# Performance work log

Measured on AMD Instinct MI355X. Metric: run time of the kernel, lower is better.

The kernel has to match this reference:

```python
import jax, jax.numpy as jnp
from jax import lax
import numpy as np


def conv2d(x, w, b, stride=1, pad=0):
    # x: [B,C,H,W], w: [O,I,kh,kw]
    y = lax.conv_general_dilated(
        x, w, (stride, stride), [(pad, pad), (pad, pad)],
        dimension_numbers=("NCHW", "OIHW", "NCHW"))
    return y + b[None, :, None, None]


def setup_inputs() -> dict:
    key = jax.random.key(0)
    ks = jax.random.split(key, 9)
    B, C, Ci, H, W = 1, 64, 32, 96, 96
    sc3 = 1.0 / np.sqrt(C * 9)   # fan-in scale for 3x3 convs
    sc1 = 1.0 / np.sqrt(C)       # fan-in scale for 1x1 convs
    scw = 1.0 / np.sqrt(Ci)
    return {
        "x":    jax.random.normal(ks[0], (B, C, H, W), jnp.float32),
        "d1_w": jax.random.normal(ks[1], (C, C, 3, 3), jnp.float32) * sc3,
        "d1_b": jnp.zeros((C,), jnp.float32),
        "d2_w": jax.random.normal(ks[2], (C, C, 3, 3), jnp.float32) * sc3,
        "d2_b": jnp.zeros((C,), jnp.float32),
        "d3_w": jax.random.normal(ks[3], (C, C, 3, 3), jnp.float32) * sc3,
        "d3_b": jnp.zeros((C,), jnp.float32),
        "g_w":  jax.random.normal(ks[4], (Ci, C, 1, 1), jnp.float32) * sc1,
        "g_b":  jnp.zeros((Ci,), jnp.float32),
        "th_w": jax.random.normal(ks[5], (Ci, C, 1, 1), jnp.float32) * sc1,
        "th_b": jnp.zeros((Ci,), jnp.float32),
        "ph_w": jax.random.normal(ks[6], (Ci, C, 1, 1), jnp.float32) * sc1,
        "ph_b": jnp.zeros((Ci,), jnp.float32),
        "W_w":  jax.random.normal(ks[7], (C, Ci, 1, 1), jnp.float32) * scw,
        "W_b":  jnp.zeros((C,), jnp.float32),
    }


def reference(x, d1_w, d1_b, d2_w, d2_b, d3_w, d3_b,
              g_w, g_b, th_w, th_b, ph_w, ph_b, W_w, W_b):
    lrelu = lambda v: jnp.where(v >= 0, v, 0.2 * v)
    y = lrelu(conv2d(x, d1_w, d1_b, stride=2, pad=1))
    y = lrelu(conv2d(y, d2_w, d2_b, stride=2, pad=1))
    y = conv2d(y, d3_w, d3_b, stride=2, pad=1)
    y = jax.image.resize(y, x.shape, method="bilinear")  # align_corners=False semantics
    x = jax.nn.sigmoid(y) * x
    # --- non-local block ---
    B, C, H, W = x.shape
    Ci = g_w.shape[0]
    gx = conv2d(x, g_w, g_b).reshape(B, Ci, -1)    # [B,Ci,N]
    tx = conv2d(x, th_w, th_b).reshape(B, Ci, -1)  # [B,Ci,N]
    px = conv2d(x, ph_w, ph_b).reshape(B, Ci, -1)  # [B,Ci,N]
    # f[b,n,m] = sum_c theta[b,n,c] * phi[b,c,m]  (N x N scores, no scaling)
    f = jnp.einsum("bcn,bcm->bnm", tx, px)
    f = jax.nn.softmax(f, axis=1)  # unconventional: softmax over FIRST token axis
    # y[b,c,n] = sum_m f[b,n,m] * g[b,c,m]
    y2 = jnp.einsum("bnm,bcm->bcn", f, gx).reshape(B, Ci, H, W)
    return conv2d(y2, W_w, W_b) + x
```

## Files before the change

### kernel.cpp

```cpp
#include <hip/hip_runtime.h>
#include <math.h>

#define NTOK 9216
#define CIN  32
#define CC   64
#define NCH1 16
#define NT1S 36
#define NCH2 12
#define MS2  24
#define LOG2E 1.4426950408889634f
#define C1INIT (-17.312340490667560f)
#define C2INIT (-9.3123404906675595f)

typedef _Float16 half8 __attribute__((ext_vector_type(8)));
typedef float    f32x4 __attribute__((ext_vector_type(4)));

static __device__ __forceinline__ float fexp2(float x) {
#if __has_builtin(__builtin_amdgcn_exp2f)
    return __builtin_amdgcn_exp2f(x);
#else
    return exp2f(x);
#endif
}

__global__ void conv3x3_quad96(const float* __restrict__ in, const float* __restrict__ w,
                               float* __restrict__ outp) {
    const int t = threadIdx.x;
    const int q = t % 12, ohl = t / 12;
    const int oh = blockIdx.x * 16 + ohl;
    const int oc = blockIdx.y, grp = blockIdx.z;
    const int ci0 = grp * 8;
    float a0 = 0.f, a1 = 0.f, a2 = 0.f, a3 = 0.f;
    const int iwl = 8 * q - 1;
    #pragma unroll
    for (int ci = 0; ci < 8; ++ci) {
        const float* ip = in + (ci0 + ci) * 96 * 96;
        const float* wp = w + oc * CC * 9 + (ci0 + ci) * 9;
        #pragma unroll
        for (int kh = 0; kh < 3; ++kh) {
            int ih = oh * 2 - 1 + kh;
            if (ih < 0) continue;
            const float* rp = ip + ih * 96;
            float ls = (q > 0) ? rp[iwl] : 0.f;
            float4 fa = *(const float4*)(rp + 8 * q);
            float4 fb = *(const float4*)(rp + 8 * q + 4);
            float w0 = wp[kh * 3], w1 = wp[kh * 3 + 1], w2 = wp[kh * 3 + 2];
            a0 = fmaf(ls,   w0, fmaf(fa.x, w1, fmaf(fa.y, w2, a0)));
            a1 = fmaf(fa.y, w0, fmaf(fa.z, w1, fmaf(fa.w, w2, a1)));
            a2 = fmaf(fa.w, w0, fmaf(fb.x, w1, fmaf(fb.y, w2, a2)));
            a3 = fmaf(fb.y, w0, fmaf(fb.z, w1, fmaf(fb.w, w2, a3)));
        }
    }
    float4 r = make_float4(a0, a1, a2, a3);
    *(float4*)(outp + grp * (CC * 2304) + oc * 2304 + oh * 48 + 4 * q) = r;
}

template<int HIN, int HOUT, int CIG>
__global__ void conv3x3_part(const float* __restrict__ in, const float* __restrict__ w,
                             float* __restrict__ outp) {
    const int p = blockIdx.x * blockDim.x + threadIdx.x;
    if (p >= HOUT * HOUT) return;
    const int oc = blockIdx.y, grp = blockIdx.z;
    const int oh = p / HOUT, ow = p % HOUT;
    const int ci0 = grp * CIG;
    float acc = 0.f;
    #pragma unroll
    for (int ci = 0; ci < CIG; ++ci) {
        const float* ip = in + (ci0 + ci) * HIN * HIN;
        const float* wp = w + oc * CC * 9 + (ci0 + ci) * 9;
        #pragma unroll
        for (int kh = 0; kh < 3; ++kh) {
            int ih = oh * 2 - 1 + kh;
            bool okh = (unsigned)ih < (unsigned)HIN;
            #pragma unroll
            for (int kw = 0; kw < 3; ++kw) {
                int iw = ow * 2 - 1 + kw;
                float v = (okh && (unsigned)iw < (unsigned)HIN) ? ip[ih * HIN + iw] : 0.f;
                acc = fmaf(v, wp[kh * 3 + kw], acc);
            }
        }
    }
    outp[grp * (CC * HOUT * HOUT) + oc * HOUT * HOUT + p] = acc;
}

template<int NG, int HW, int LRELU>
__global__ void conv_merge(const float* __restrict__ parts, const float* __restrict__ b,
                           float* __restrict__ out) {
    int idx = blockIdx.x * 256 + threadIdx.x;
    int oc = idx / HW;
    float acc = b[oc];
    #pragma unroll
    for (int g = 0; g < NG; ++g)
        acc += parts[g * (CC * HW) + idx];
    if (LRELU) acc = acc >= 0.f ? acc : 0.2f * acc;
    out[idx] = acc;
}

__global__ void gate_kernel(const float* __restrict__ x, const float* __restrict__ y3,
                            float* __restrict__ xg) {
    int idx = blockIdx.x * 256 + threadIdx.x;
    int c = idx / (96 * 96);
    int p = idx % (96 * 96);
    int h = p / 96, w = p % 96;
    float fh = (h + 0.5f) * 0.125f - 0.5f;
    float fw = (w + 0.5f) * 0.125f - 0.5f;
    int h0 = (int)floorf(fh); float ah = fh - (float)h0;
    int w0 = (int)floorf(fw); float aw = fw - (float)w0;
    int h0c = min(max(h0, 0), 11), h1c = min(max(h0 + 1, 0), 11);
    int w0c = min(max(w0, 0), 11), w1c = min(max(w0 + 1, 0), 11);
    const float* yp = y3 + c * 144;
    float v = (1.f - ah) * ((1.f - aw) * yp[h0c * 12 + w0c] + aw * yp[h0c * 12 + w1c])
            +         ah * ((1.f - aw) * yp[h1c * 12 + w0c] + aw * yp[h1c * 12 + w1c]);
    float sg = 1.f / (1.f + __expf(-v));
    xg[idx] = sg * x[idx];
}

__global__ void conv1x1_fused(const float* __restrict__ xg,
                              const float* __restrict__ gw, const float* __restrict__ gb,
                              const float* __restrict__ thw, const float* __restrict__ thb,
                              const float* __restrict__ phw, const float* __restrict__ phb,
                              float* __restrict__ gx, float* __restrict__ tx,
                              float* __restrict__ px) {
    int ci = blockIdx.y;
    int n = blockIdx.x * 256 + threadIdx.x;
    float ag = gb[ci], at = thb[ci], ap = phb[ci];
    #pragma unroll 8
    for (int c = 0; c < CC; ++c) {
        float v = xg[c * NTOK + n];
        ag = fmaf(gw[ci * CC + c],  v, ag);
        at = fmaf(thw[ci * CC + c], v, at);
        ap = fmaf(phw[ci * CC + c], v, ap);
    }
    gx[ci * NTOK + n] = ag;
    tx[ci * NTOK + n] = at * LOG2E;
    px[ci * NTOK + n] = ap;
}

__global__ void repackAB(const float* __restrict__ tx, const float* __restrict__ px,
                         _Float16* __restrict__ txF, _Float16* __restrict__ pxF) {
    const float* src = blockIdx.y ? px : tx;
    _Float16* dst    = blockIdx.y ? pxF : txF;
    int gid = blockIdx.x * 256 + threadIdx.x;
    int t = gid >> 6, l = gid & 63;
    int n = t * 16 + (l & 15);
    int khi = (l >> 4) * 4;
    half8 v;
    #pragma unroll
    for (int e = 0; e < 8; ++e) {
        int c = (e >> 2) * 16 + khi + (e & 3);
        v[e] = (_Float16)src[c * NTOK + n];
    }
    *(half8*)(dst + gid * 8) = v;
}

__global__ __launch_bounds__(256) void phase1(const _Float16* __restrict__ txF,
                                              const _Float16* __restrict__ pxF,
                                              float* __restrict__ Dp) {
    int w = threadIdx.x >> 6, l = threadIdx.x & 63;
    int mtile0 = (blockIdx.x * 4 + w) * 4;
    half8 pf[4];
    #pragma unroll
    for (int j = 0; j < 4; ++j)
        pf[j] = *(const half8*)(pxF + (mtile0 + j) * 512 + l * 8);
    f32x4 cini = {C1INIT, C1INIT, C1INIT, C1INIT};
    float dsum[4][4] = {};
    int nt0 = blockIdx.y * NT1S;
    for (int i = 0; i < NT1S; ++i) {
        half8 tf = *(const half8*)(txF + (nt0 + i) * 512 + l * 8);
        #pragma unroll
        for (int j = 0; j < 4; ++j) {
            f32x4 s = __builtin_amdgcn_mfma_f32_16x16x32_f16(pf[j], tf, cini, 0, 0, 0);
            #pragma unroll
            for (int r = 0; r < 4; ++r)
                dsum[j][r] += fexp2(s[r]);
        }
    }
    #pragma unroll
    for (int off = 1; off < 16; off <<= 1)
        #pragma unroll
        for (int j = 0; j < 4; ++j)
            #pragma unroll
            for (int r = 0; r < 4; ++r)
                dsum[j][r] += __shfl_xor(dsum[j][r], off);
    if ((l & 15) == 0) {
        #pragma unroll
        for (int j = 0; j < 4; ++j) {
            int m = (mtile0 + j) * 16 + (l >> 4) * 4;
            #pragma unroll
            for (int r = 0; r < 4; ++r)
                Dp[blockIdx.y * NTOK + m + r] = dsum[j][r];
        }
    }
}

__global__ void repackG(const float* __restrict__ gx, const float* __restrict__ Dp,
                        _Float16* __restrict__ gxF) {
    __shared__ float lds[CIN][65];
    __shared__ float idl[64];
    int m0 = blockIdx.x * 64;
    int tid = threadIdx.x;
    for (int idx = tid; idx < CIN * 64; idx += 256)
        lds[idx >> 6][idx & 63] = gx[(idx >> 6) * NTOK + m0 + (idx & 63)];
    if (tid < 64) {
        float D = 0.f;
        #pragma unroll
        for (int ch = 0; ch < NCH1; ++ch) D += Dp[ch * NTOK + m0 + tid];
        idl[tid] = 1.0f / D;
    }
    __syncthreads();
    int mt = tid >> 7;
    int slot = tid & 127;
    int ct = slot >> 6;
    int l  = slot & 63;
    int khi = (l >> 4) * 4;
    int c = ct * 16 + (l & 15);
    half8 v;
    #pragma unroll
    for (int e = 0; e < 8; ++e) {
        int mloc = mt * 32 + (e >> 2) * 16 + khi + (e & 3);
        v[e] = (_Float16)(lds[c][mloc] * idl[mloc]);
    }
    int tile = (blockIdx.x * 2 + mt) * 2 + ct;
    *(half8*)(gxF + tile * 512 + l * 8) = v;
}

__global__ __launch_bounds__(256) void phase2(const _Float16* __restrict__ txF,
                                              const _Float16* __restrict__ pxF,
                                              const _Float16* __restrict__ gxF,
                                              float* __restrict__ y2p) {
    int w = threadIdx.x >> 6, l = threadIdx.x & 63;
    int ntile0 = (blockIdx.x * 4 + w) * 4;
    half8 tf[4];
    #pragma unroll
    for (int j = 0; j < 4; ++j)
        tf[j] = *(const half8*)(txF + (ntile0 + j) * 512 + l * 8);
    int khi = (l >> 4) * 4;
    f32x4 zero = {0.f, 0.f, 0.f, 0.f};
    f32x4 cini = {C2INIT, C2INIT, C2INIT, C2INIT};
    f32x4 acc[4][2];
    #pragma unroll
    for (int j = 0; j < 4; ++j) { acc[j][0] = zero; acc[j][1] = zero; }
    int mbase = blockIdx.y * (NTOK / NCH2);
    for (int ms = 0; ms < MS2; ++ms) {
        int m0 = mbase + ms * 32;
        int mt16 = m0 >> 4;
        half8 pf0 = *(const half8*)(pxF + mt16 * 512 + l * 8);
        half8 pf1 = *(const half8*)(pxF + (mt16 + 1) * 512 + l * 8);
        int gt = (m0 >> 5) * 2;
        half8 gf0 = *(const half8*)(gxF + gt * 512 + l * 8);
        half8 gf1 = *(const half8*)(gxF + (gt + 1) * 512 + l * 8);
        #pragma unroll
        for (int j = 0; j < 4; ++j) {
            f32x4 s0 = __builtin_amdgcn_mfma_f32_16x16x32_f16(pf0, tf[j], cini, 0, 0, 0);
            f32x4 s1 = __builtin_amdgcn_mfma_f32_16x16x32_f16(pf1, tf[j], cini, 0, 0, 0);
            half8 ff;
            #pragma unroll
            for (int r = 0; r < 4; ++r) {
                ff[r]     = (_Float16)fexp2(s0[r]);
                ff[4 + r] = (_Float16)fexp2(s1[r]);
            }
            acc[j][0] = __builtin_amdgcn_mfma_f32_16x16x32_f16(ff, gf0, acc[j][0], 0, 0, 0);
            acc[j][1] = __builtin_amdgcn_mfma_f32_16x16x32_f16(ff, gf1, acc[j][1], 0, 0, 0);
        }
    }
    float* base = y2p + blockIdx.y * (CIN * NTOK);
    #pragma unroll
    for (int j = 0; j < 4; ++j) {
        int n = (ntile0 + j) * 16 + khi;
        #pragma unroll
        for (int r = 0; r < 4; ++r) {
            base[(l & 15) * NTOK + n + r]        = acc[j][0][r] * 0.00390625f;
            base[(16 + (l & 15)) * NTOK + n + r] = acc[j][1][r] * 0.00390625f;
        }
    }
}

__global__ void mergeY2(const float* __restrict__ y2p, float* __restrict__ att) {
    int idx = blockIdx.x * 256 + threadIdx.x;
    float s = 0.f;
    #pragma unroll
    for (int ch = 0; ch < NCH2; ++ch) s += y2p[ch * (CIN * NTOK) + idx];
    att[idx] = s;
}

__global__ void final_conv(const float* __restrict__ att, const float* __restrict__ Ww,
                           const float* __restrict__ Wb, const float* __restrict__ xg,
                           float* __restrict__ out) {
    int co = blockIdx.y;
    int n = blockIdx.x * 256 + threadIdx.x;
    float acc = Wb[co];
    #pragma unroll
    for (int ci = 0; ci < CIN; ++ci)
        acc = fmaf(Ww[co * CIN + ci], att[ci * NTOK + n], acc);
    out[co * NTOK + n] = acc + xg[co * NTOK + n];
}

extern "C" void kernel_launch(void* const* d_in, const int* in_sizes, int n_in,
                              void* d_out, int out_size, void* d_ws, size_t ws_size,
                              hipStream_t stream) {
    const float* x   = (const float*)d_in[0];
    const float* d1w = (const float*)d_in[1];  const float* d1b = (const float*)d_in[2];
    const float* d2w = (const float*)d_in[3];  const float* d2b = (const float*)d_in[4];
    const float* d3w = (const float*)d_in[5];  const float* d3b = (const float*)d_in[6];
    const float* gw  = (const float*)d_in[7];  const float* gb  = (const float*)d_in[8];
    const float* thw = (const float*)d_in[9];  const float* thb = (const float*)d_in[10];
    const float* phw = (const float*)d_in[11]; const float* phb = (const float*)d_in[12];
    const float* Ww  = (const float*)d_in[13]; const float* Wb  = (const float*)d_in[14];
    float* out = (float*)d_out;

    float* W    = (float*)d_ws;
    float* xg   = W;
    float* y1   = W + 589824;
    float* y2c  = W + 737280;
    float* y3   = W + 774144;
    float* txb  = W + 783360;
    float* pxb  = W + 1078272;
    float* gxb  = W + 1373184;
    float* Dp   = W + 1668096;
    float* att  = W + 1815552;
    float* y2p  = W + 2110464;
    _Float16* txF = (_Float16*)(W + 5649408);
    _Float16* pxF = (_Float16*)(W + 5796864);
    _Float16* gxF = (_Float16*)(W + 5944320);

    float* cp1 = y2p;
    float* cp2 = y2p + 1179648;
    float* cp3 = y2p + 1769472;

    conv3x3_quad96<<<dim3(3, CC, 8), 192, 0, stream>>>(x, d1w, cp1);
    conv_merge<8, 2304, 1><<<576, 256, 0, stream>>>(cp1, d1b, y1);
    conv3x3_part<48, 24, 4><<<dim3(3, CC, 16), 192, 0, stream>>>(y1,  d2w, cp2);
    conv_merge<16, 576, 1><<<144, 256, 0, stream>>>(cp2, d2b, y2c);
    conv3x3_part<24, 12, 4><<<dim3(1, CC, 16), 192, 0, stream>>>(y2c, d3w, cp3);
    conv_merge<16, 144, 0><<<36, 256, 0, stream>>>(cp3, d3b, y3);
    gate_kernel<<<2304, 256, 0, stream>>>(x, y3, xg);

    conv1x1_fused<<<dim3(36, CIN), 256, 0, stream>>>(xg, gw, gb, thw, thb, phw, phb,
                                                     gxb, txb, pxb);
    repackAB<<<dim3(144, 2), 256, 0, stream>>>(txb, pxb, txF, pxF);

    phase1<<<dim3(36, NCH1), 256, 0, stream>>>(txF, pxF, Dp);
    repackG<<<144, 256, 0, stream>>>(gxb, Dp, gxF);
    phase2<<<dim3(36, NCH2), 256, 0, stream>>>(txF, pxF, gxF, y2p);
    mergeY2<<<1152, 256, 0, stream>>>(y2p, att);

    final_conv<<<dim3(36, CC), 256, 0, stream>>>(att, Ww, Wb, xg, out);
}
```

Before: 122.3 us.

## Fuse fp16 fragment repacking into 1x1 conv and fold softmax normalizer into phase2

The 1x1 projection kernel now writes theta, phi and g directly as fp16 in the MFMA fragment layout, which removes the separate repackAB and repackG kernels and their fp32 intermediate buffers. The softmax column normalizer is no longer multiplied into g; phase2 sums the Dp partials itself and subtracts log2(D) from the MFMA accumulator init, so the exponent already carries the normalization. The merge kernels (conv_merge, mergeY2) are vectorized to float4 with correspondingly fewer blocks. In exchange, the fused conv writes scattered 2-byte stores, and every phase2 block recomputes its slice of D.

```diff
diff --git a/kernel.cpp b/kernel.cpp
--- a/kernel.cpp
+++ b/kernel.cpp
@@ -8,6 +8,7 @@
 #define NT1S 36
 #define NCH2 12
 #define MS2  24
+#define MCH2 768
 #define LOG2E 1.4426950408889634f
 #define C1INIT (-17.312340490667560f)
 #define C2INIT (-9.3123404906675595f)
@@ -34,7 +35,7 @@
     const int iwl = 8 * q - 1;
     #pragma unroll
     for (int ci = 0; ci < 8; ++ci) {
-        const float* ip = in + (ci0 + ci) * 96 * 96;
+        const float* ip = in + (ci0 + ci) * 9216;
         const float* wp = w + oc * CC * 9 + (ci0 + ci) * 9;
         #pragma unroll
         for (int kh = 0; kh < 3; ++kh) {
@@ -84,43 +85,53 @@
 }
 
 template<int NG, int HW, int LRELU>
-__global__ void conv_merge(const float* __restrict__ parts, const float* __restrict__ b,
-                           float* __restrict__ out) {
-    int idx = blockIdx.x * 256 + threadIdx.x;
-    int oc = idx / HW;
-    float acc = b[oc];
-    #pragma unroll
-    for (int g = 0; g < NG; ++g)
-        acc += parts[g * (CC * HW) + idx];
-    if (LRELU) acc = acc >= 0.f ? acc : 0.2f * acc;
-    out[idx] = acc;
-}
-
-__global__ void gate_kernel(const float* __restrict__ x, const float* __restrict__ y3,
-                            float* __restrict__ xg) {
-    int idx = blockIdx.x * 256 + threadIdx.x;
-    int c = idx / (96 * 96);
-    int p = idx % (96 * 96);
-    int h = p / 96, w = p % 96;
+__global__ void conv_merge4(const float* __restrict__ parts, const float* __restrict__ b,
+                            float* __restrict__ out) {
+    int i4 = blockIdx.x * 256 + threadIdx.x;
+    int oc = (i4 * 4) / HW;
+    float bb = b[oc];
+    float4 acc = make_float4(bb, bb, bb, bb);
+    #pragma unroll
+    for (int g = 0; g < NG; ++g) {
+        float4 p = *(const float4*)(parts + g * (CC * HW) + i4 * 4);
+        acc.x += p.x; acc.y += p.y; acc.z += p.z; acc.w += p.w;
+    }
+    if (LRELU) {
+        acc.x = acc.x >= 0.f ? acc.x : 0.2f * acc.x;
+        acc.y = acc.y >= 0.f ? acc.y : 0.2f * acc.y;
+        acc.z = acc.z >= 0.f ? acc.z : 0.2f * acc.z;
+        acc.w = acc.w >= 0.f ? acc.w : 0.2f * acc.w;
+    }
+    *(float4*)(out + i4 * 4) = acc;
+}
+
+static __device__ __forceinline__ float gate_val(const float* __restrict__ y3c, int n) {
+    int h = n / 96, wc = n % 96;
     float fh = (h + 0.5f) * 0.125f - 0.5f;
-    float fw = (w + 0.5f) * 0.125f - 0.5f;
+    float fw = (wc + 0.5f) * 0.125f - 0.5f;
     int h0 = (int)floorf(fh); float ah = fh - (float)h0;
     int w0 = (int)floorf(fw); float aw = fw - (float)w0;
     int h0c = min(max(h0, 0), 11), h1c = min(max(h0 + 1, 0), 11);
     int w0c = min(max(w0, 0), 11), w1c = min(max(w0 + 1, 0), 11);
-    const float* yp = y3 + c * 144;
-    float v = (1.f - ah) * ((1.f - aw) * yp[h0c * 12 + w0c] + aw * yp[h0c * 12 + w1c])
-            +         ah * ((1.f - aw) * yp[h1c * 12 + w0c] + aw * yp[h1c * 12 + w1c]);
-    float sg = 1.f / (1.f + __expf(-v));
+    float v = (1.f - ah) * ((1.f - aw) * y3c[h0c * 12 + w0c] + aw * y3c[h0c * 12 + w1c])
+            +         ah * ((1.f - aw) * y3c[h1c * 12 + w0c] + aw * y3c[h1c * 12 + w1c]);
+    return 1.f / (1.f + __expf(-v));
+}
+
+__global__ void gate_kernel(const float* __restrict__ x, const float* __restrict__ y3,
+                            float* __restrict__ xg) {
+    int idx = blockIdx.x * 256 + threadIdx.x;
+    int c = idx / 9216, n = idx % 9216;
+    float sg = gate_val(y3 + c * 144, n);
     xg[idx] = sg * x[idx];
 }
 
-__global__ void conv1x1_fused(const float* __restrict__ xg,
-                              const float* __restrict__ gw, const float* __restrict__ gb,
-                              const float* __restrict__ thw, const float* __restrict__ thb,
-                              const float* __restrict__ phw, const float* __restrict__ phb,
-                              float* __restrict__ gx, float* __restrict__ tx,
-                              float* __restrict__ px) {
+__global__ void conv1x1_frag(const float* __restrict__ xg,
+                             const float* __restrict__ gw, const float* __restrict__ gb,
+                             const float* __restrict__ thw, const float* __restrict__ thb,
+                             const float* __restrict__ phw, const float* __restrict__ phb,
+                             _Float16* __restrict__ txF, _Float16* __restrict__ pxF,
+                             _Float16* __restrict__ gxF) {
     int ci = blockIdx.y;
     int n = blockIdx.x * 256 + threadIdx.x;
     float ag = gb[ci], at = thb[ci], ap = phb[ci];
@@ -131,26 +142,14 @@
         at = fmaf(thw[ci * CC + c], v, at);
         ap = fmaf(phw[ci * CC + c], v, ap);
     }
-    gx[ci * NTOK + n] = ag;
-    tx[ci * NTOK + n] = at * LOG2E;
-    px[ci * NTOK + n] = ap;
-}
-
-__global__ void repackAB(const float* __restrict__ tx, const float* __restrict__ px,
-                         _Float16* __restrict__ txF, _Float16* __restrict__ pxF) {
-    const float* src = blockIdx.y ? px : tx;
-    _Float16* dst    = blockIdx.y ? pxF : txF;
-    int gid = blockIdx.x * 256 + threadIdx.x;
-    int t = gid >> 6, l = gid & 63;
-    int n = t * 16 + (l & 15);
-    int khi = (l >> 4) * 4;
-    half8 v;
-    #pragma unroll
-    for (int e = 0; e < 8; ++e) {
-        int c = (e >> 2) * 16 + khi + (e & 3);
-        v[e] = (_Float16)src[c * NTOK + n];
-    }
-    *(half8*)(dst + gid * 8) = v;
+    int addr_ab = (n >> 4) * 512 + (((n & 15) | (((ci & 15) >> 2) << 4)) * 8)
+                + (((ci >> 4) << 2) | (ci & 3));
+    txF[addr_ab] = (_Float16)(at * LOG2E);
+    pxF[addr_ab] = (_Float16)ap;
+    int addr_g = ((n >> 5) * 2 + (ci >> 4)) * 512
+               + (((ci & 15) | (((n & 15) >> 2) << 4)) * 8)
+               + ((((n >> 4) & 1) << 2) | (n & 3));
+    gxF[addr_g] = (_Float16)ag;
 }
 
 __global__ __launch_bounds__(256) void phase1(const _Float16* __restrict__ txF,
@@ -193,41 +192,20 @@
     }
 }
 
-__global__ void repackG(const float* __restrict__ gx, const float* __restrict__ Dp,
-                        _Float16* __restrict__ gxF) {
-    __shared__ float lds[CIN][65];
-    __shared__ float idl[64];
-    int m0 = blockIdx.x * 64;
-    int tid = threadIdx.x;
-    for (int idx = tid; idx < CIN * 64; idx += 256)
-        lds[idx >> 6][idx & 63] = gx[(idx >> 6) * NTOK + m0 + (idx & 63)];
-    if (tid < 64) {
-        float D = 0.f;
-        #pragma unroll
-        for (int ch = 0; ch < NCH1; ++ch) D += Dp[ch * NTOK + m0 + tid];
-        idl[tid] = 1.0f / D;
-    }
-    __syncthreads();
-    int mt = tid >> 7;
-    int slot = tid & 127;
-    int ct = slot >> 6;
-    int l  = slot & 63;
-    int khi = (l >> 4) * 4;
-    int c = ct * 16 + (l & 15);
-    half8 v;
-    #pragma unroll
-    for (int e = 0; e < 8; ++e) {
-        int mloc = mt * 32 + (e >> 2) * 16 + khi + (e & 3);
-        v[e] = (_Float16)(lds[c][mloc] * idl[mloc]);
-    }
-    int tile = (blockIdx.x * 2 + mt) * 2 + ct;
-    *(half8*)(gxF + tile * 512 + l * 8) = v;
-}
-
 __global__ __launch_bounds__(256) void phase2(const _Float16* __restrict__ txF,
                                               const _Float16* __restrict__ pxF,
                                               const _Float16* __restrict__ gxF,
+                                              const float* __restrict__ Dp,
                                               float* __restrict__ y2p) {
+    __shared__ float l2D[MCH2];
+    int mbase = blockIdx.y * MCH2;
+    for (int i = threadIdx.x; i < MCH2; i += 256) {
+        float D = 0.f;
+        #pragma unroll
+        for (int ch = 0; ch < NCH1; ++ch) D += Dp[ch * NTOK + mbase + i];
+        l2D[i] = __log2f(D);
+    }
+    __syncthreads();
     int w = threadIdx.x >> 6, l = threadIdx.x & 63;
     int ntile0 = (blockIdx.x * 4 + w) * 4;
     half8 tf[4];
@@ -236,23 +214,27 @@
         tf[j] = *(const half8*)(txF + (ntile0 + j) * 512 + l * 8);
     int khi = (l >> 4) * 4;
     f32x4 zero = {0.f, 0.f, 0.f, 0.f};
-    f32x4 cini = {C2INIT, C2INIT, C2INIT, C2INIT};
+    f32x4 c2v = {C2INIT, C2INIT, C2INIT, C2INIT};
     f32x4 acc[4][2];
     #pragma unroll
     for (int j = 0; j < 4; ++j) { acc[j][0] = zero; acc[j][1] = zero; }
-    int mbase = blockIdx.y * (NTOK / NCH2);
     for (int ms = 0; ms < MS2; ++ms) {
         int m0 = mbase + ms * 32;
+        int mloc = ms * 32;
         int mt16 = m0 >> 4;
         half8 pf0 = *(const half8*)(pxF + mt16 * 512 + l * 8);
         half8 pf1 = *(const half8*)(pxF + (mt16 + 1) * 512 + l * 8);
+        f32x4 l2a = *(const f32x4*)&l2D[mloc + khi];
+        f32x4 l2b = *(const f32x4*)&l2D[mloc + 16 + khi];
+        f32x4 cini0 = c2v - l2a;
+        f32x4 cini1 = c2v - l2b;
         int gt = (m0 >> 5) * 2;
         half8 gf0 = *(const half8*)(gxF + gt * 512 + l * 8);
         half8 gf1 = *(const half8*)(gxF + (gt + 1) * 512 + l * 8);
         #pragma unroll
         for (int j = 0; j < 4; ++j) {
-            f32x4 s0 = __builtin_amdgcn_mfma_f32_16x16x32_f16(pf0, tf[j], cini, 0, 0, 0);
-            f32x4 s1 = __builtin_amdgcn_mfma_f32_16x16x32_f16(pf1, tf[j], cini, 0, 0, 0);
+            f32x4 s0 = __builtin_amdgcn_mfma_f32_16x16x32_f16(pf0, tf[j], cini0, 0, 0, 0);
+            f32x4 s1 = __builtin_amdgcn_mfma_f32_16x16x32_f16(pf1, tf[j], cini1, 0, 0, 0);
             half8 ff;
             #pragma unroll
             for (int r = 0; r < 4; ++r) {
@@ -276,11 +258,14 @@
 }
 
 __global__ void mergeY2(const float* __restrict__ y2p, float* __restrict__ att) {
-    int idx = blockIdx.x * 256 + threadIdx.x;
-    float s = 0.f;
-    #pragma unroll
-    for (int ch = 0; ch < NCH2; ++ch) s += y2p[ch * (CIN * NTOK) + idx];
-    att[idx] = s;
+    int i4 = blockIdx.x * 256 + threadIdx.x;
+    float4 s = make_float4(0.f, 0.f, 0.f, 0.f);
+    #pragma unroll
+    for (int ch = 0; ch < NCH2; ++ch) {
+        float4 p = *(const float4*)(y2p + ch * (CIN * NTOK) + i4 * 4);
+        s.x += p.x; s.y += p.y; s.z += p.z; s.w += p.w;
+    }
+    *(float4*)(att + i4 * 4) = s;
 }
 
 __global__ void final_conv(const float* __restrict__ att, const float* __restrict__ Ww,
@@ -313,36 +298,31 @@
     float* y1   = W + 589824;
     float* y2c  = W + 737280;
     float* y3   = W + 774144;
-    float* txb  = W + 783360;
-    float* pxb  = W + 1078272;
-    float* gxb  = W + 1373184;
-    float* Dp   = W + 1668096;
-    float* att  = W + 1815552;
-    float* y2p  = W + 2110464;
-    _Float16* txF = (_Float16*)(W + 5649408);
-    _Float16* pxF = (_Float16*)(W + 5796864);
-    _Float16* gxF = (_Float16*)(W + 5944320);
+    float* Dp   = W + 783360;
+    float* att  = W + 930816;
+    float* y2p  = W + 1225728;
+    _Float16* txF = (_Float16*)(W + 4764672);
+    _Float16* pxF = (_Float16*)(W + 4912128);
+    _Float16* gxF = (_Float16*)(W + 5059584);
 
     float* cp1 = y2p;
     float* cp2 = y2p + 1179648;
     float* cp3 = y2p + 1769472;
 
     conv3x3_quad96<<<dim3(3, CC, 8), 192, 0, stream>>>(x, d1w, cp1);
-    conv_merge<8, 2304, 1><<<576, 256, 0, stream>>>(cp1, d1b, y1);
-    conv3x3_part<48, 24, 4><<<dim3(3, CC, 16), 192, 0, stream>>>(y1,  d2w, cp2);
-    conv_merge<16, 576, 1><<<144, 256, 0, stream>>>(cp2, d2b, y2c);
+    conv_merge4<8, 2304, 1><<<144, 256, 0, stream>>>(cp1, d1b, y1);
+    conv3x3_part<48, 24, 4><<<dim3(3, CC, 16), 192, 0, stream>>>(y1, d2w, cp2);
+    conv_merge4<16, 576, 1><<<36, 256, 0, stream>>>(cp2, d2b, y2c);
     conv3x3_part<24, 12, 4><<<dim3(1, CC, 16), 192, 0, stream>>>(y2c, d3w, cp3);
-    conv_merge<16, 144, 0><<<36, 256, 0, stream>>>(cp3, d3b, y3);
+    conv_merge4<16, 144, 0><<<9, 256, 0, stream>>>(cp3, d3b, y3);
     gate_kernel<<<2304, 256, 0, stream>>>(x, y3, xg);
 
-    conv1x1_fused<<<dim3(36, CIN), 256, 0, stream>>>(xg, gw, gb, thw, thb, phw, phb,
-                                                     gxb, txb, pxb);
-    repackAB<<<dim3(144, 2), 256, 0, stream>>>(txb, pxb, txF, pxF);
+    conv1x1_frag<<<dim3(36, CIN), 256, 0, stream>>>(xg, gw, gb, thw, thb, phw, phb,
+                                                    txF, pxF, gxF);
 
     phase1<<<dim3(36, NCH1), 256, 0, stream>>>(txF, pxF, Dp);
-    repackG<<<144, 256, 0, stream>>>(gxb, Dp, gxF);
-    phase2<<<dim3(36, NCH2), 256, 0, stream>>>(txF, pxF, gxF, y2p);
-    mergeY2<<<1152, 256, 0, stream>>>(y2p, att);
+    phase2<<<dim3(36, NCH2), 256, 0, stream>>>(txF, pxF, gxF, Dp, y2p);
+    mergeY2<<<288, 256, 0, stream>>>(y2p, att);
 
     final_conv<<<dim3(36, CC), 256, 0, stream>>>(att, Ww, Wb, xg, out);
 }
```

Result: no change. 120.7 us (-1.3%).
